# Kernel tuning notes

Hardware: AMD Instinct MI355X
Metric: run time of the kernel (lower is better)

## Reference

```python
import jax, jax.numpy as jnp
import numpy as np

WINDOW = 127          # odd
W = (WINDOW - 1) // 2 # 63 half-window
Q_CH = WINDOW + 1     # 128 query chunk
K_CH = WINDOW * 2     # 254 key chunk


def _compl_mod(m, n):
    return int(n * int(np.ceil(m / n)) - m)


def setup_inputs() -> dict:
    key = jax.random.key(0)
    kq, kk, kv = jax.random.split(key, 3)
    B, L, NH, H = 4, 4096, 16, 64
    return {
        "q": jax.random.normal(kq, (B, L, NH, H), dtype=jnp.float32),
        "k": jax.random.normal(kk, (B, L, NH, H), dtype=jnp.float32),
        "v": jax.random.normal(kv, (B, L, NH, H), dtype=jnp.float32),
    }


def _build_mask(c, k_pad, dtype_bool=bool):
    # base band mask over one (q_ch, k_ch) block: True = masked out
    u = jnp.triu(jnp.ones((Q_CH, K_CH), dtype=bool))
    band = jnp.logical_and(u, jnp.flip(u, (0, 1)))
    base = ~band
    mask_left = base.at[:, :W].set(True)
    mask_right = base.at[:, K_CH - (W + k_pad):].set(True)
    if c > 1:
        mid = jnp.broadcast_to(base, (c - 2, Q_CH, K_CH)) if c > 2 else jnp.zeros((0, Q_CH, K_CH), bool)
        return jnp.concatenate([mask_left[None], mid, mask_right[None]], axis=0)
    return jnp.logical_or(mask_left, mask_right)[None]


def reference(q, k, v):
    b, s, nh, h = q.shape
    q = q * (h ** -0.5)

    q_pad = _compl_mod(s, Q_CH)
    k_pad = _compl_mod(s + 2 * W - K_CH, Q_CH)

    # chunk queries: (b, c, q_ch, nh, h)
    qp = jnp.pad(q, ((0, 0), (0, q_pad), (0, 0), (0, 0)))
    c = (s + q_pad) // Q_CH
    qw = qp.reshape(b, c, Q_CH, nh, h)

    # overlapping key/value windows via gather: (b, c, k_ch, nh, h)
    kp = jnp.pad(k, ((0, 0), (W, W + k_pad), (0, 0), (0, 0)))
    vp = jnp.pad(v, ((0, 0), (W, W + k_pad), (0, 0), (0, 0)))
    starts = np.arange(c) * Q_CH
    idx = starts[:, None] + np.arange(K_CH)[None, :]  # (c, k_ch)
    kw = kp[:, idx]
    vw = vp[:, idx]

    # block scores: (b, nh, c, q_ch, k_ch)
    A = jnp.einsum('bcqnh,bcknh->bncqk', qw, kw)

    mask = _build_mask(c, k_pad)  # (c, q_ch, k_ch)
    neg = -jnp.finfo(A.dtype).max
    A = jnp.where(mask[None, None], neg, A)
    A = jax.nn.softmax(A, axis=-1)

    z = jnp.einsum('bncqk,bcknh->bncqh', A, vw)  # (b, nh, c, q_ch, h)
    z = z.reshape(b, nh, c * Q_CH, h)[:, :, :s]
    return jnp.transpose(z, (0, 2, 1, 3))  # (b, s, nh, h)
```

## Files before the change

kernel.cpp:

```cpp
#include <hip/hip_runtime.h>


typedef _Float16 f16;
typedef _Float16 f16x2  __attribute__((ext_vector_type(2)));
typedef _Float16 f16x4  __attribute__((ext_vector_type(4)));
typedef _Float16 f16x8  __attribute__((ext_vector_type(8)));
typedef float    f32x16 __attribute__((ext_vector_type(16)));
typedef int      int4v  __attribute__((ext_vector_type(4)));

constexpr int NB = 4, L = 4096, NH = 16, H = 64;
constexpr int CQ = 128, NC = L / CQ, KW = 256, WR = 63;
constexpr int RS = NH * H;

constexpr int Q_OFF = 0;
constexpr int K_OFF = 16384;
constexpr int V_OFF = 49152;
constexpr int LDS_BYTES = 81920;

#define DEV static __device__ __forceinline__

DEV int iclamp(int x, int lo, int hi) { return x < lo ? lo : (x > hi ? hi : x); }

DEV float fexp2(float x) {
#if __has_builtin(__builtin_amdgcn_exp2f)
    return __builtin_amdgcn_exp2f(x);
#else
    return exp2f(x);
#endif
}

DEV int packh2(float a, float b) {
    f16x2 p; p.x = (f16)a; p.y = (f16)b;
    return __builtin_bit_cast(int, p);
}

DEV int rmaddr(int base, int r, int colb) {
    return base + r * 128 + (colb ^ ((r & 7) << 4));
}

DEV int vaddr(int h, int kb) {
    return V_OFF + ((h * 512 + kb) ^ ((((h & 7) ^ ((h >> 3) & 7))) << 4));
}

DEV int oaddr(int row, int col) {
    return (row * 64 + col) ^ ((row & 3) << 2);
}

DEV void swap_halves(int& a, int& b, int hi) {
    int pa = __shfl_xor(a, 32, 64);
    int pb = __shfl_xor(b, 32, 64);
    int na = hi ? pb : a;
    int nb = hi ? b  : pa;
    a = na; b = nb;
}

__global__ __launch_bounds__(512, 4)
void wattn_kernel(const float* __restrict__ q_, const float* __restrict__ k_,
                  const float* __restrict__ v_, float* __restrict__ o_)
{
    __shared__ alignas(16) char smem[LDS_BYTES];
    float* O_lds = (float*)smem;
    float* D_lds = (float*)(smem + 32768);

    const int bid = (int)blockIdx.x;
    const int wid = (bid & 7) * ((NB * NH * NC) / 8) + (bid >> 3);
    const int c = wid & (NC - 1);
    const int n = (wid >> 5) & (NH - 1);
    const int b = wid >> 9;

    const int t    = (int)threadIdx.x;
    const int lane = t & 63;
    const int w    = t >> 6;
    const int lq   = lane & 31;
    const int hi   = lane >> 5;
    const int qt   = w & 3;
    const int half = w >> 2;

    const int kg0 = c * CQ - WR;
    const size_t bn = ((size_t)b * L * NH + n) * H;
    const float qs = 0.125f * 1.44269504088896f;

    const int h4 = (t & 15) << 2;
    const int cb = h4 << 1;
    const int ru = t >> 4;

    {
        const float* qp = q_ + bn + (size_t)(c * CQ) * RS + h4;
        #pragma unroll
        for (int p = 0; p < 4; ++p) {
            int r = ru + p * 32;
            float4 x = *(const float4*)(qp + (size_t)r * RS);
            *(f16x4*)(smem + rmaddr(Q_OFF, r, cb)) =
                (f16x4){(f16)(x.x * qs), (f16)(x.y * qs), (f16)(x.z * qs), (f16)(x.w * qs)};
        }
    }
    #pragma unroll
    for (int p = 0; p < 8; ++p) {
        int r  = ru + p * 32;
        int kr = iclamp(kg0 + r, 0, L - 1);
        float4 x = *(const float4*)(k_ + bn + (size_t)kr * RS + h4);
        *(f16x4*)(smem + rmaddr(K_OFF, r, cb)) =
            (f16x4){(f16)x.x, (f16)x.y, (f16)x.z, (f16)x.w};
    }
    #pragma unroll
    for (int p = 0; p < 4; ++p) {
        int r0  = ru * 2 + p * 64;
        int kr0 = iclamp(kg0 + r0,     0, L - 1);
        int kr1 = iclamp(kg0 + r0 + 1, 0, L - 1);
        float4 v0 = *(const float4*)(v_ + bn + (size_t)kr0 * RS + h4);
        float4 v1 = *(const float4*)(v_ + bn + (size_t)kr1 * RS + h4);
        int kb = r0 * 2;
        *(f16x2*)(smem + vaddr(h4 + 0, kb)) = (f16x2){(f16)v0.x, (f16)v1.x};
        *(f16x2*)(smem + vaddr(h4 + 1, kb)) = (f16x2){(f16)v0.y, (f16)v1.y};
        *(f16x2*)(smem + vaddr(h4 + 2, kb)) = (f16x2){(f16)v0.z, (f16)v1.z};
        *(f16x2*)(smem + vaddr(h4 + 3, kb)) = (f16x2){(f16)v0.w, (f16)v1.w};
    }

    const int iq  = qt * 32 + lq;
    const int jlo = (c == 0) ? WR : 0;
    const int jhi = (KW < L - kg0) ? KW : (L - kg0);
    const int lo  = (iq > jlo) ? iq : jlo;
    const int hb  = (iq + 126 < jhi - 1) ? (iq + 126) : (jhi - 1);
    const unsigned span = (unsigned)(hb - lo);

    f32x16 o0, o1;
    #pragma unroll
    for (int r = 0; r < 16; ++r) { o0[r] = 0.f; o1[r] = 0.f; }
    float dsum = 0.f;

    __syncthreads();

    f16x8 qf[4];
    #pragma unroll
    for (int tq = 0; tq < 4; ++tq)
        qf[tq] = *(const f16x8*)(smem + rmaddr(Q_OFF, qt * 32 + lq, 32 * tq + 16 * hi));

    auto body = [&](int kt) {
        f16x8 kf[4];
        #pragma unroll
        for (int tq = 0; tq < 4; ++tq)
            kf[tq] = *(const f16x8*)(smem + rmaddr(K_OFF, kt * 32 + lq, 32 * tq + 16 * hi));

        f32x16 s;
        #pragma unroll
        for (int r = 0; r < 16; ++r) s[r] = 0.f;
        #pragma unroll
        for (int tq = 0; tq < 4; ++tq)
            s = __builtin_amdgcn_mfma_f32_32x32x16_f16(kf[tq], qf[tq], s, 0, 0, 0);

        const int jb = kt * 32 + 4 * hi;
        float pe[16];
        #pragma unroll
        for (int r = 0; r < 16; ++r) {
            int j = jb + (r & 3) + ((r >> 2) << 3);
            float e = fexp2(s[r]);
            e = ((unsigned)(j - lo) <= span) ? e : 0.f;
            dsum += e;
            pe[r] = e;
        }
        int d0 = packh2(pe[0],  pe[1]),  d1 = packh2(pe[2],  pe[3]);
        int d2 = packh2(pe[4],  pe[5]),  d3 = packh2(pe[6],  pe[7]);
        int d4 = packh2(pe[8],  pe[9]),  d5 = packh2(pe[10], pe[11]);
        int d6 = packh2(pe[12], pe[13]), d7 = packh2(pe[14], pe[15]);
        swap_halves(d0, d2, hi); swap_halves(d1, d3, hi);
        swap_halves(d4, d6, hi); swap_halves(d5, d7, hi);
        f16x8 pa0 = __builtin_bit_cast(f16x8, (int4v){d0, d1, d2, d3});
        f16x8 pa1 = __builtin_bit_cast(f16x8, (int4v){d4, d5, d6, d7});

        const int kb = kt * 64 + hi * 16;
        f16x8 vb00 = *(const f16x8*)(smem + vaddr(lq,      kb));
        f16x8 vb01 = *(const f16x8*)(smem + vaddr(lq,      kb + 32));
        f16x8 vb10 = *(const f16x8*)(smem + vaddr(32 + lq, kb));
        f16x8 vb11 = *(const f16x8*)(smem + vaddr(32 + lq, kb + 32));
        o0 = __builtin_amdgcn_mfma_f32_32x32x16_f16(pa0, vb00, o0, 0, 0, 0);
        o0 = __builtin_amdgcn_mfma_f32_32x32x16_f16(pa1, vb01, o0, 0, 0, 0);
        o1 = __builtin_amdgcn_mfma_f32_32x32x16_f16(pa0, vb10, o1, 0, 0, 0);
        o1 = __builtin_amdgcn_mfma_f32_32x32x16_f16(pa1, vb11, o1, 0, 0, 0);
    };

    const int kt0 = qt + half * 3;
    body(kt0);
    body(kt0 + 1);
    if (!half) body(kt0 + 2);

    float dw = dsum + __shfl_xor(dsum, 32, 64);

    __syncthreads();

    if (half) {
        #pragma unroll
        for (int r = 0; r < 16; ++r) {
            int qloc = (r & 3) + ((r >> 2) << 3) + 4 * hi;
            int row  = qt * 32 + qloc;
            O_lds[oaddr(row, lq)]      = o0[r];
            O_lds[oaddr(row, 32 + lq)] = o1[r];
        }
        if (lane < 32) D_lds[qt * 32 + lq] = dw;
    }
    __syncthreads();

    if (!half) {
        float dinv = 1.0f / (dw + D_lds[iq]);
        #pragma unroll
        for (int r = 0; r < 16; ++r) {
            int qloc = (r & 3) + ((r >> 2) << 3) + 4 * hi;
            int row  = qt * 32 + qloc;
            float rd = __shfl(dinv, qloc, 64);
            int a0 = oaddr(row, lq), a1 = oaddr(row, 32 + lq);
            O_lds[a0] = (o0[r] + O_lds[a0]) * rd;
            O_lds[a1] = (o1[r] + O_lds[a1]) * rd;
        }
    }
    __syncthreads();

    const size_t ob = ((size_t)b * L + (size_t)c * CQ) * RS + (size_t)n * H;
    #pragma unroll
    for (int it = 0; it < 4; ++it) {
        int flat = it * 512 + t;
        int row  = flat >> 4;
        int hh   = (flat & 15) << 2;
        float4 val = *(const float4*)(O_lds + oaddr(row, hh));
        *(float4*)(o_ + ob + (size_t)row * RS + hh) = val;
    }
}

extern "C" void kernel_launch(void* const* d_in, const int* in_sizes, int n_in,
                              void* d_out, int out_size, void* d_ws, size_t ws_size,
                              hipStream_t stream) {
    const float* q = (const float*)d_in[0];
    const float* k = (const float*)d_in[1];
    const float* v = (const float*)d_in[2];
    float* o = (float*)d_out;
    (void)in_sizes; (void)n_in; (void)out_size; (void)d_ws; (void)ws_size;
    wattn_kernel<<<dim3(NB * NH * NC), dim3(512), 0, stream>>>(q, k, v, o);
}
```

Measured before the change: 49.92 us.

## Transpose PV MFMA output and write results directly from registers

Swaps the MFMA operand order so the PV accumulator holds output transposed, with each lane owning one query row and several head dims. The combine step then stores the non-half partials to LDS transposed, and the other half adds, normalizes with its own per-lane reciprocal and writes float4s straight to global memory. This removes one barrier, the LDS staging pass and the per-row shuffles. It also replaces the shfl-based half swap with the v_permlane32_swap instruction. Each lane now writes its own row to global memory, so stores are less coalesced than the previous staged writes, and the inline asm ties the kernel to hardware that provides that instruction.

```diff
diff --git a/kernel.cpp b/kernel.cpp
--- a/kernel.cpp
+++ b/kernel.cpp
@@ -42,16 +42,8 @@
     return V_OFF + ((h * 512 + kb) ^ ((((h & 7) ^ ((h >> 3) & 7))) << 4));
 }
 
-DEV int oaddr(int row, int col) {
-    return (row * 64 + col) ^ ((row & 3) << 2);
-}
-
-DEV void swap_halves(int& a, int& b, int hi) {
-    int pa = __shfl_xor(a, 32, 64);
-    int pb = __shfl_xor(b, 32, 64);
-    int na = hi ? pb : a;
-    int nb = hi ? b  : pa;
-    a = na; b = nb;
+DEV void swap_halves(int& a, int& b) {
+    asm volatile("v_permlane32_swap_b32 %0, %1" : "+v"(a), "+v"(b));
 }
 
 __global__ __launch_bounds__(512, 4)
@@ -162,8 +154,8 @@
         int d2 = packh2(pe[4],  pe[5]),  d3 = packh2(pe[6],  pe[7]);
         int d4 = packh2(pe[8],  pe[9]),  d5 = packh2(pe[10], pe[11]);
         int d6 = packh2(pe[12], pe[13]), d7 = packh2(pe[14], pe[15]);
-        swap_halves(d0, d2, hi); swap_halves(d1, d3, hi);
-        swap_halves(d4, d6, hi); swap_halves(d5, d7, hi);
+        swap_halves(d0, d2); swap_halves(d1, d3);
+        swap_halves(d4, d6); swap_halves(d5, d7);
         f16x8 pa0 = __builtin_bit_cast(f16x8, (int4v){d0, d1, d2, d3});
         f16x8 pa1 = __builtin_bit_cast(f16x8, (int4v){d4, d5, d6, d7});
 
@@ -172,10 +164,10 @@
         f16x8 vb01 = *(const f16x8*)(smem + vaddr(lq,      kb + 32));
         f16x8 vb10 = *(const f16x8*)(smem + vaddr(32 + lq, kb));
         f16x8 vb11 = *(const f16x8*)(smem + vaddr(32 + lq, kb + 32));
-        o0 = __builtin_amdgcn_mfma_f32_32x32x16_f16(pa0, vb00, o0, 0, 0, 0);
-        o0 = __builtin_amdgcn_mfma_f32_32x32x16_f16(pa1, vb01, o0, 0, 0, 0);
-        o1 = __builtin_amdgcn_mfma_f32_32x32x16_f16(pa0, vb10, o1, 0, 0, 0);
-        o1 = __builtin_amdgcn_mfma_f32_32x32x16_f16(pa1, vb11, o1, 0, 0, 0);
+        o0 = __builtin_amdgcn_mfma_f32_32x32x16_f16(vb00, pa0, o0, 0, 0, 0);
+        o0 = __builtin_amdgcn_mfma_f32_32x32x16_f16(vb01, pa1, o0, 0, 0, 0);
+        o1 = __builtin_amdgcn_mfma_f32_32x32x16_f16(vb10, pa0, o1, 0, 0, 0);
+        o1 = __builtin_amdgcn_mfma_f32_32x32x16_f16(vb11, pa1, o1, 0, 0, 0);
     };
 
     const int kt0 = qt + half * 3;
@@ -187,40 +179,36 @@
 
     __syncthreads();
 
+    if (!half) {
+        #pragma unroll
+        for (int r = 0; r < 16; ++r) {
+            int h = (r & 3) + ((r >> 2) << 3) + 4 * hi;
+            O_lds[h * 128 + iq]        = o0[r];
+            O_lds[(32 + h) * 128 + iq] = o1[r];
+        }
+        if (lane < 32) D_lds[iq] = dw;
+    }
+    __syncthreads();
+
     if (half) {
-        #pragma unroll
-        for (int r = 0; r < 16; ++r) {
-            int qloc = (r & 3) + ((r >> 2) << 3) + 4 * hi;
-            int row  = qt * 32 + qloc;
-            O_lds[oaddr(row, lq)]      = o0[r];
-            O_lds[oaddr(row, 32 + lq)] = o1[r];
-        }
-        if (lane < 32) D_lds[qt * 32 + lq] = dw;
-    }
-    __syncthreads();
-
-    if (!half) {
         float dinv = 1.0f / (dw + D_lds[iq]);
-        #pragma unroll
-        for (int r = 0; r < 16; ++r) {
-            int qloc = (r & 3) + ((r >> 2) << 3) + 4 * hi;
-            int row  = qt * 32 + qloc;
-            float rd = __shfl(dinv, qloc, 64);
-            int a0 = oaddr(row, lq), a1 = oaddr(row, 32 + lq);
-            O_lds[a0] = (o0[r] + O_lds[a0]) * rd;
-            O_lds[a1] = (o1[r] + O_lds[a1]) * rd;
-        }
-    }
-    __syncthreads();
-
-    const size_t ob = ((size_t)b * L + (size_t)c * CQ) * RS + (size_t)n * H;
-    #pragma unroll
-    for (int it = 0; it < 4; ++it) {
-        int flat = it * 512 + t;
-        int row  = flat >> 4;
-        int hh   = (flat & 15) << 2;
-        float4 val = *(const float4*)(O_lds + oaddr(row, hh));
-        *(float4*)(o_ + ob + (size_t)row * RS + hh) = val;
+        const size_t ob = ((size_t)b * L + (size_t)c * CQ) * RS + (size_t)n * H;
+        float* orow = o_ + ob + (size_t)iq * RS;
+        #pragma unroll
+        for (int m = 0; m < 4; ++m) {
+            int h0 = 8 * m + 4 * hi;
+            float4 v0, v1;
+            v0.x = (o0[4 * m + 0] + O_lds[(h0 + 0) * 128 + iq]) * dinv;
+            v0.y = (o0[4 * m + 1] + O_lds[(h0 + 1) * 128 + iq]) * dinv;
+            v0.z = (o0[4 * m + 2] + O_lds[(h0 + 2) * 128 + iq]) * dinv;
+            v0.w = (o0[4 * m + 3] + O_lds[(h0 + 3) * 128 + iq]) * dinv;
+            v1.x = (o1[4 * m + 0] + O_lds[(32 + h0 + 0) * 128 + iq]) * dinv;
+            v1.y = (o1[4 * m + 1] + O_lds[(32 + h0 + 1) * 128 + iq]) * dinv;
+            v1.z = (o1[4 * m + 2] + O_lds[(32 + h0 + 2) * 128 + iq]) * dinv;
+            v1.w = (o1[4 * m + 3] + O_lds[(32 + h0 + 3) * 128 + iq]) * dinv;
+            *(float4*)(orow + h0)      = v0;
+            *(float4*)(orow + 32 + h0) = v1;
+        }
     }
 }
 
```

Result: no change. 50.51 us (+1.2%).
